# Kernel optimization log

Hardware: AMD Instinct MI355X
Metric: run time of the kernel (lower is better)

## Reference

```python
import jax, jax.numpy as jnp
import numpy as np

B, T, I, H, O = 4096, 512, 1, 64, 1


def setup_inputs() -> dict:
    key = jax.random.key(0)
    ks = jax.random.split(key, 7)
    s = 1.0 / np.sqrt(H)  # PyTorch default init scale
    return {
        "x": jax.random.normal(ks[0], (B, T, I), dtype=jnp.float32),
        "w_ih": jax.random.uniform(ks[1], (4 * H, I), jnp.float32, -s, s),
        "w_hh": jax.random.uniform(ks[2], (4 * H, H), jnp.float32, -s, s),
        "b_ih": jax.random.uniform(ks[3], (4 * H,), jnp.float32, -s, s),
        "b_hh": jax.random.uniform(ks[4], (4 * H,), jnp.float32, -s, s),
        "w_out": jax.random.uniform(ks[5], (O, H), jnp.float32, -s, s),
        "b_out": jax.random.uniform(ks[6], (O,), jnp.float32, -s, s),
    }


def reference(x, w_ih, w_hh, b_ih, b_hh, w_out, b_out):
    # x: [B, T, I]; PyTorch gate order in 4H dim is (i, f, g, o)
    b = b_ih + b_hh  # [4H]
    # precompute input projections for all timesteps: [T, B, 4H]
    xg = jnp.einsum("bti,gi->tbg", x, w_ih) + b

    def step(carry, xg_t):
        h, c = carry  # [B, H] each
        gates = xg_t + h @ w_hh.T  # [B, 4H]
        i, f, g, o = jnp.split(gates, 4, axis=-1)
        i = jax.nn.sigmoid(i)
        f = jax.nn.sigmoid(f)
        g = jnp.tanh(g)
        o = jax.nn.sigmoid(o)
        c = f * c + i * g
        h = o * jnp.tanh(c)
        return (h, c), None

    nb = x.shape[0]
    h0 = jnp.zeros((nb, w_hh.shape[1]), x.dtype)
    (h_T, _), _ = jax.lax.scan(step, (h0, h0), xg)
    # linear on last hidden state only (lstm_out[:, -1, :])
    return h_T @ w_out.T + b_out
```

## Files before the change

kernel.cpp:

```cpp
#include <hip/hip_runtime.h>


#define TT   512
#define MB   8
#define HP   72
#define BUFE (16 * HP)
#define SXP  10

typedef _Float16 f16x8 __attribute__((ext_vector_type(8)));
typedef float    f32x4 __attribute__((ext_vector_type(4)));

#define MFMA16(a, b, c) __builtin_amdgcn_mfma_f32_16x16x32_f16((a), (b), (c), 0, 0, 0)

__device__ __forceinline__ float rcp_(float x) { return __builtin_amdgcn_rcpf(x); }
__device__ __forceinline__ float sigmoid_(float x) { return rcp_(1.0f + __expf(-x)); }
__device__ __forceinline__ float tanh_(float x) { return 1.0f - 2.0f * rcp_(1.0f + __expf(2.0f * x)); }

__device__ __forceinline__ f16x8 cvt8(const float4& u0, const float4& u1) {
    f16x8 r;
    r[0] = (_Float16)u0.x; r[1] = (_Float16)u0.y; r[2] = (_Float16)u0.z; r[3] = (_Float16)u0.w;
    r[4] = (_Float16)u1.x; r[5] = (_Float16)u1.y; r[6] = (_Float16)u1.z; r[7] = (_Float16)u1.w;
    return r;
}

__global__ __launch_bounds__(256, 2) void lstm_mfma(
    const float* __restrict__ x,
    const float* __restrict__ w_ih,
    const float* __restrict__ w_hh,
    const float* __restrict__ b_ih,
    const float* __restrict__ b_hh,
    const float* __restrict__ w_out,
    const float* __restrict__ b_out,
    float* __restrict__ out)
{
    __shared__ __align__(16) float    sh_x[TT * SXP];
    __shared__ __align__(16) _Float16 hbuf[2 * BUFE];

    const int tid = threadIdx.x;
    const int w   = tid >> 6;
    const int L   = tid & 63;
    const int l16 = L & 15;
    const int h0  = L >> 4;
    const int b0  = blockIdx.x * MB;
    const int j   = 16 * w + l16;

    {
        const int q = tid >> 5;
        const int l = tid & 31;
        const float* xr = x + (size_t)(b0 + q) * TT;
        #pragma unroll
        for (int i = 0; i < TT / 32; ++i)
            sh_x[(l + 32 * i) * SXP + q] = xr[l + 32 * i];
    }
    for (int i = tid; i < 2 * BUFE; i += 256) hbuf[i] = (_Float16)0.0f;

    f16x8 Bf[4][2];
    float wihv[4], biasv[4];
    #pragma unroll
    for (int s = 0; s < 4; ++s) {
        const int n = 64 * s + j;
        #pragma unroll
        for (int kt = 0; kt < 2; ++kt) {
            const float* p = w_hh + n * 64 + kt * 32 + h0 * 8;
            float4 u0 = *(const float4*)p;
            float4 u1 = *(const float4*)(p + 4);
            Bf[s][kt] = cvt8(u0, u1);
        }
        wihv[s]  = w_ih[n];
        biasv[s] = b_ih[n] + b_hh[n];
    }

    const int aoff = l16 * HP + h0 * 8;
    const int xoff = 2 * h0;
    const int wr   = 4 * h0 * HP + j;

    float cc0 = 0.0f, cc1 = 0.0f;
    __syncthreads();

    if (((blockIdx.x >> 8) ^ blockIdx.x) & 1) {
        __builtin_amdgcn_s_sleep(12);
    }

    auto step = [&](const _Float16* rb, _Float16* wb, int t) {
        f16x8 a0 = *(const f16x8*)(rb + aoff);
        f16x8 a1 = *(const f16x8*)(rb + aoff + 32);
        const float2 xv = *(const float2*)(sh_x + t * SXP + xoff);

        f32x4 acc[4];
        #pragma unroll
        for (int s = 0; s < 4; ++s) {
            f32x4 ci = {fmaf(xv.x, wihv[s], biasv[s]), 0.f,
                        fmaf(xv.y, wihv[s], biasv[s]), 0.f};
            acc[s] = MFMA16(a1, Bf[s][1], MFMA16(a0, Bf[s][0], ci));
        }

        {
            float gi = acc[0][0] + acc[0][1];
            float gf = acc[1][0] + acc[1][1];
            float gg = acc[2][0] + acc[2][1];
            float go = acc[3][0] + acc[3][1];
            float i_ = sigmoid_(gi), f_ = sigmoid_(gf);
            float g_ = tanh_(gg),   o_ = sigmoid_(go);
            cc0 = fmaf(f_, cc0, i_ * g_);
            float hv = o_ * tanh_(cc0);
            _Float16 hh = (_Float16)hv;
            wb[wr]      = hh;
            wb[wr + HP] = (_Float16)(hv - (float)hh);
        }
        {
            float gi = acc[0][2] + acc[0][3];
            float gf = acc[1][2] + acc[1][3];
            float gg = acc[2][2] + acc[2][3];
            float go = acc[3][2] + acc[3][3];
            float i_ = sigmoid_(gi), f_ = sigmoid_(gf);
            float g_ = tanh_(gg),   o_ = sigmoid_(go);
            cc1 = fmaf(f_, cc1, i_ * g_);
            float hv = o_ * tanh_(cc1);
            _Float16 hh = (_Float16)hv;
            wb[wr + 2 * HP] = hh;
            wb[wr + 3 * HP] = (_Float16)(hv - (float)hh);
        }
        __syncthreads();
    };

    for (int t = 0; t < TT; t += 2) {
        step(hbuf,        hbuf + BUFE, t);
        step(hbuf + BUFE, hbuf,        t + 1);
    }

    const float wo = w_out[L];
    #pragma unroll
    for (int p = 0; p < 2; ++p) {
        const int q = 2 * w + p;
        float hvf = (float)hbuf[(2 * q) * HP + L] + (float)hbuf[(2 * q + 1) * HP + L];
        float v = hvf * wo;
        #pragma unroll
        for (int off = 32; off; off >>= 1) v += __shfl_down(v, off);
        if (L == 0) out[b0 + q] = v + b_out[0];
    }
}

extern "C" void kernel_launch(void* const* d_in, const int* in_sizes, int n_in,
                              void* d_out, int out_size, void* d_ws, size_t ws_size,
                              hipStream_t stream) {
    const float* x     = (const float*)d_in[0];
    const float* w_ih  = (const float*)d_in[1];
    const float* w_hh  = (const float*)d_in[2];
    const float* b_ih  = (const float*)d_in[3];
    const float* b_hh  = (const float*)d_in[4];
    const float* w_out = (const float*)d_in[5];
    const float* b_out = (const float*)d_in[6];
    float* out = (float*)d_out;

    lstm_mfma<<<4096 / MB, 256, 0, stream>>>(x, w_ih, w_hh, b_ih, b_hh,
                                             w_out, b_out, out);
}
```

Measured before the change: 319.3 us.

## Fold log2e scaling into weights and share reciprocals across gate activations

Pre-scales the recurrent weights, input weights and biases by -log2(e) (or 2*log2(e) for the g gate) so that the gate pre-activations feed exp2 directly, with no per-step multiply. The i/f/g activations are combined into a single reciprocal of their product, and the o gate and tanh(c) share a second reciprocal. This cuts the per-cell transcendental count from five rcp to two. The next step's input-projection constants are computed after the MFMAs are issued, which takes them off the critical path. The s_sleep stagger is also shortened. In exchange, products of denominators risk overflow (the c term is clamped) and fp16-rounding the scaled weights changes numerics slightly.

```diff
diff --git a/kernel.cpp b/kernel.cpp
--- a/kernel.cpp
+++ b/kernel.cpp
@@ -7,19 +7,23 @@
 #define BUFE (16 * HP)
 #define SXP  10
 
+#define L2E  1.4426950408889634f
+#define L2E2 2.8853900817779268f
+
 typedef _Float16 f16x8 __attribute__((ext_vector_type(8)));
 typedef float    f32x4 __attribute__((ext_vector_type(4)));
 
 #define MFMA16(a, b, c) __builtin_amdgcn_mfma_f32_16x16x32_f16((a), (b), (c), 0, 0, 0)
 
-__device__ __forceinline__ float rcp_(float x) { return __builtin_amdgcn_rcpf(x); }
-__device__ __forceinline__ float sigmoid_(float x) { return rcp_(1.0f + __expf(-x)); }
-__device__ __forceinline__ float tanh_(float x) { return 1.0f - 2.0f * rcp_(1.0f + __expf(2.0f * x)); }
+__device__ __forceinline__ float rcp_(float x)  { return __builtin_amdgcn_rcpf(x); }
+__device__ __forceinline__ float exp2_(float x) { return __builtin_amdgcn_exp2f(x); }
 
-__device__ __forceinline__ f16x8 cvt8(const float4& u0, const float4& u1) {
+__device__ __forceinline__ f16x8 cvt8s(const float4& u0, const float4& u1, float s) {
     f16x8 r;
-    r[0] = (_Float16)u0.x; r[1] = (_Float16)u0.y; r[2] = (_Float16)u0.z; r[3] = (_Float16)u0.w;
-    r[4] = (_Float16)u1.x; r[5] = (_Float16)u1.y; r[6] = (_Float16)u1.z; r[7] = (_Float16)u1.w;
+    r[0] = (_Float16)(u0.x * s); r[1] = (_Float16)(u0.y * s);
+    r[2] = (_Float16)(u0.z * s); r[3] = (_Float16)(u0.w * s);
+    r[4] = (_Float16)(u1.x * s); r[5] = (_Float16)(u1.y * s);
+    r[6] = (_Float16)(u1.z * s); r[7] = (_Float16)(u1.w * s);
     return r;
 }
 
@@ -54,6 +58,7 @@
     }
     for (int i = tid; i < 2 * BUFE; i += 256) hbuf[i] = (_Float16)0.0f;
 
+    const float sc[4] = {-L2E, -L2E, L2E2, -L2E};
     f16x8 Bf[4][2];
     float wihv[4], biasv[4];
     #pragma unroll
@@ -64,10 +69,10 @@
             const float* p = w_hh + n * 64 + kt * 32 + h0 * 8;
             float4 u0 = *(const float4*)p;
             float4 u1 = *(const float4*)(p + 4);
-            Bf[s][kt] = cvt8(u0, u1);
+            Bf[s][kt] = cvt8s(u0, u1, sc[s]);
         }
-        wihv[s]  = w_ih[n];
-        biasv[s] = b_ih[n] + b_hh[n];
+        wihv[s]  = w_ih[n] * sc[s];
+        biasv[s] = (b_ih[n] + b_hh[n]) * sc[s];
     }
 
     const int aoff = l16 * HP + h0 * 8;
@@ -75,47 +80,69 @@
     const int wr   = 4 * h0 * HP + j;
 
     float cc0 = 0.0f, cc1 = 0.0f;
+
+    auto cellup = [&](float ai, float af, float ag, float ao, float& cc) -> float {
+        float Ei = exp2_(ai), Ef = exp2_(af), Eg = exp2_(ag);
+        float Di = 1.0f + Ei, Df = 1.0f + Ef, Dg = 1.0f + Eg;
+        float Pif = Di * Df;
+        float u   = rcp_(Pif * Dg);
+        float si  = u * (Df * Dg);
+        float sf  = u * (Di * Dg);
+        float tg  = fmaf(-2.0f, u * Pif, 1.0f);
+        cc = fmaf(sf, cc, si * tg);
+        float Ec = exp2_(fminf(cc * L2E2, 64.0f));
+        float Eo = exp2_(ao);
+        float Dc = 1.0f + Ec, Do = 1.0f + Eo;
+        float u2 = rcp_(Do * Dc);
+        return (u2 * Dc) * fmaf(-2.0f, u2 * Do, 1.0f);
+    };
+
+    f32x4 ci[4];
+    {
+        const float2 x0 = *(const float2*)(sh_x + 0 * SXP + xoff);
+        #pragma unroll
+        for (int s = 0; s < 4; ++s) {
+            ci[s][0] = fmaf(x0.x, wihv[s], biasv[s]);
+            ci[s][1] = 0.0f;
+            ci[s][2] = fmaf(x0.y, wihv[s], biasv[s]);
+            ci[s][3] = 0.0f;
+        }
+    }
+
     __syncthreads();
 
     if (((blockIdx.x >> 8) ^ blockIdx.x) & 1) {
-        __builtin_amdgcn_s_sleep(12);
+        __builtin_amdgcn_s_sleep(10);
     }
 
     auto step = [&](const _Float16* rb, _Float16* wb, int t) {
         f16x8 a0 = *(const f16x8*)(rb + aoff);
         f16x8 a1 = *(const f16x8*)(rb + aoff + 32);
-        const float2 xv = *(const float2*)(sh_x + t * SXP + xoff);
 
         f32x4 acc[4];
         #pragma unroll
-        for (int s = 0; s < 4; ++s) {
-            f32x4 ci = {fmaf(xv.x, wihv[s], biasv[s]), 0.f,
-                        fmaf(xv.y, wihv[s], biasv[s]), 0.f};
-            acc[s] = MFMA16(a1, Bf[s][1], MFMA16(a0, Bf[s][0], ci));
+        for (int s = 0; s < 4; ++s)
+            acc[s] = MFMA16(a1, Bf[s][1], MFMA16(a0, Bf[s][0], ci[s]));
+
+        if (t + 1 < TT) {
+            const float2 xn = *(const float2*)(sh_x + (t + 1) * SXP + xoff);
+            #pragma unroll
+            for (int s = 0; s < 4; ++s) {
+                ci[s][0] = fmaf(xn.x, wihv[s], biasv[s]);
+                ci[s][2] = fmaf(xn.y, wihv[s], biasv[s]);
+            }
         }
 
         {
-            float gi = acc[0][0] + acc[0][1];
-            float gf = acc[1][0] + acc[1][1];
-            float gg = acc[2][0] + acc[2][1];
-            float go = acc[3][0] + acc[3][1];
-            float i_ = sigmoid_(gi), f_ = sigmoid_(gf);
-            float g_ = tanh_(gg),   o_ = sigmoid_(go);
-            cc0 = fmaf(f_, cc0, i_ * g_);
-            float hv = o_ * tanh_(cc0);
+            float hv = cellup(acc[0][0] + acc[0][1], acc[1][0] + acc[1][1],
+                              acc[2][0] + acc[2][1], acc[3][0] + acc[3][1], cc0);
             _Float16 hh = (_Float16)hv;
             wb[wr]      = hh;
             wb[wr + HP] = (_Float16)(hv - (float)hh);
         }
         {
-            float gi = acc[0][2] + acc[0][3];
-            float gf = acc[1][2] + acc[1][3];
-            float gg = acc[2][2] + acc[2][3];
-            float go = acc[3][2] + acc[3][3];
-            float i_ = sigmoid_(gi), f_ = sigmoid_(gf);
-            float g_ = tanh_(gg),   o_ = sigmoid_(go);
-            cc1 = fmaf(f_, cc1, i_ * g_);
-            float hv = o_ * tanh_(cc1);
+            float hv = cellup(acc[0][2] + acc[0][3], acc[1][2] + acc[1][3],
+                              acc[2][2] + acc[2][3], acc[3][2] + acc[3][3], cc1);
             _Float16 hh = (_Float16)hv;
             wb[wr + 2 * HP] = hh;
             wb[wr + 3 * HP] = (_Float16)(hv - (float)hh);
```

Result: slower. 328.8 us (+3.0%).
